# Optimization experiments

Measured on AMD Instinct MI355X. Metric: run time of the kernel, lower is better.

## Reference

```python
import jax, jax.numpy as jnp
import numpy as np


def conv1x1(x, W, b):
    # 1x1 Conv2d == per-pixel linear over channels. x: [B,C,H,W], W: [O,C], b: [O]
    return jnp.einsum('oc,bchw->bohw', W, x) + b[None, :, None, None]


def setup_inputs() -> dict:
    key = jax.random.key(0)
    ks = jax.random.split(key, 18)
    B, C, Hd, H, W = 16, 64, 64, 32, 32
    s = 0.05
    f = jax.random.normal
    return {
        'h': f(ks[0], (B, C, H, W), jnp.float32),
        'm': f(ks[1], (B, C, H, W), jnp.float32),
        'Wq': f(ks[2], (Hd, C), jnp.float32) * s,
        'bq': f(ks[3], (Hd,), jnp.float32) * s,
        'Wk': f(ks[4], (Hd, C), jnp.float32) * s,
        'bk': f(ks[5], (Hd,), jnp.float32) * s,
        'Wk2': f(ks[6], (Hd, C), jnp.float32) * s,
        'bk2': f(ks[7], (Hd,), jnp.float32) * s,
        'Wv': f(ks[8], (C, C), jnp.float32) * s,
        'bv': f(ks[9], (C,), jnp.float32) * s,
        'Wv2': f(ks[10], (C, C), jnp.float32) * s,
        'bv2': f(ks[11], (C,), jnp.float32) * s,
        'Wz': f(ks[12], (2 * C, 2 * C), jnp.float32) * s,
        'bz': f(ks[13], (2 * C,), jnp.float32) * s,
        'Wm': f(ks[14], (3 * C, 3 * C), jnp.float32) * s,
        'bm': f(ks[15], (3 * C,), jnp.float32) * s,
    }


def reference(h, m, Wq, bq, Wk, bk, Wk2, bk2, Wv, bv, Wv2, bv2, Wz, bz, Wm, bm):
    B, C, H, W = h.shape
    Hd = Wq.shape[0]
    N = H * W
    # Shared query from h
    Q_h = conv1x1(h, Wq, bq).reshape(B, Hd, N).transpose(0, 2, 1)  # [B,N,Hd]
    # Self-attention branch over h
    K_h = conv1x1(h, Wk, bk).reshape(B, Hd, N)                     # [B,Hd,N]
    A_h = jax.nn.softmax(jnp.einsum('bnd,bdm->bnm', Q_h, K_h), axis=-1)  # [B,N,N]
    V_h = conv1x1(h, Wv, bv).reshape(B, C, N)                      # [B,C,N]
    Z_h = jnp.einsum('bnm,bcm->bcn', A_h, V_h).reshape(B, C, H, W)
    # Cross-attention branch over memory m (same query Q_h)
    K_m = conv1x1(m, Wk2, bk2).reshape(B, Hd, N)
    A_m = jax.nn.softmax(jnp.einsum('bnd,bdm->bnm', Q_h, K_m), axis=-1)
    V_m = conv1x1(m, Wv2, bv2).reshape(B, C, N)
    Z_m = jnp.einsum('bnm,bcm->bcn', A_m, V_m).reshape(B, C, H, W)
    # Fuse and gated memory update
    Z = conv1x1(jnp.concatenate([Z_h, Z_m], axis=1), Wz, bz)       # [B,2C,H,W]
    combined = conv1x1(jnp.concatenate([Z, h], axis=1), Wm, bm)    # [B,3C,H,W]
    mo, mg, mi = combined[:, :C], combined[:, C:2 * C], combined[:, 2 * C:]
    mi = jax.nn.sigmoid(mi)
    new_m = (1 - mi) * m + mi * jnp.tanh(mg)
    new_h = jax.nn.sigmoid(mo) * new_m
    return (new_h, new_m)
```

## Files before the change

kernel.cpp:

```cpp
#include <hip/hip_runtime.h>

typedef unsigned short u16;
typedef unsigned int u32;
typedef __attribute__((ext_vector_type(8))) short bf16x8;
typedef __attribute__((ext_vector_type(4))) float f32x4;

#define MFMA(a, b, c) __builtin_amdgcn_mfma_f32_16x16x32_bf16((a), (b), (c), 0, 0, 0)

static __device__ __forceinline__ u16 f2bf(float x) {
  u32 u = __float_as_uint(x);
  u += 0x7FFFu + ((u >> 16) & 1u);
  return (u16)(u >> 16);
}
static __device__ __forceinline__ u16 f2bf_t(float x) {
  return (u16)(__float_as_uint(x) >> 16);
}

__global__ void prep_kernel(const float* __restrict__ Wq, const float* __restrict__ Wk,
                            const float* __restrict__ Wk2, const float* __restrict__ Wv,
                            const float* __restrict__ Wv2, const float* __restrict__ Wz,
                            const float* __restrict__ Wm, const float* __restrict__ bm,
                            u16* __restrict__ W5, u16* __restrict__ Wzb,
                            u16* __restrict__ Wmb, float* __restrict__ bmp) {
  const int id = blockIdx.x * 256 + threadIdx.x;
  if (id < 20480) {
    const int wi = id >> 12, e = id & 4095;
    const float* src = wi == 0 ? Wq : wi == 1 ? Wk : wi == 2 ? Wk2 : wi == 3 ? Wv : Wv2;
    W5[id] = f2bf(src[e]);
  } else if (id < 36864) {
    const int e = id - 20480;
    Wzb[e] = f2bf(Wz[e]);
  } else if (id < 73728) {
    const int e = id - 36864;
    const int p = e / 192, k = e % 192;
    const int hb2 = p / 96, r1 = p % 96, ctl = r1 / 48, r2 = r1 % 48;
    const int g = r2 >> 4, mm = r2 & 15;
    const int o = g * 64 + (hb2 * 2 + ctl) * 16 + mm;
    Wmb[p * 192 + k] = f2bf(Wm[o * 192 + k]);
  } else if (id < 73920) {
    const int p = id - 73728;
    const int hb2 = p / 96, r1 = p % 96, ctl = r1 / 48, r2 = r1 % 48;
    const int g = r2 >> 4, mm = r2 & 15;
    const int o = g * 64 + (hb2 * 2 + ctl) * 16 + mm;
    bmp[p] = bm[o];
  }
}

__global__ __launch_bounds__(256) void proj_kernel(
    const float* __restrict__ h, const float* __restrict__ m_,
    const float* __restrict__ bq, const float* __restrict__ bk,
    const float* __restrict__ bk2, const float* __restrict__ bv,
    const float* __restrict__ bv2, const u16* __restrict__ W5,
    u16* __restrict__ Qb, u16* __restrict__ Khb, u16* __restrict__ Kmb,
    u16* __restrict__ Vhb, u16* __restrict__ Vmb, u16* __restrict__ hbuf)
{
  const int b = blockIdx.y, n0 = blockIdx.x * 64, z = blockIdx.z;
  __shared__ __align__(16) u16 xt[64][72];
  __shared__ __align__(16) u16 st[64][72];
  const int tid = threadIdx.x;
  const float* __restrict__ X = z ? m_ : h;

  {
    const int px = tid & 63, c0 = tid >> 6;
#pragma unroll
    for (int i = 0; i < 16; ++i) {
      const int c = c0 * 16 + i;
      xt[px][c] = f2bf(X[(b * 64 + c) * 1024 + n0 + px]);
    }
  }
  __syncthreads();

  const int lane = tid & 63, w = tid >> 6;
  const int mm = lane & 15, q = lane >> 4;

  const bf16x8 xa0 = *(const bf16x8*)&xt[w * 16 + mm][q * 8];
  const bf16x8 xa1 = *(const bf16x8*)&xt[w * 16 + mm][32 + q * 8];

  auto gemm_tile = [&](const u16* Wb, const float* bias, int ot) -> f32x4 {
    const bf16x8 b0 = *(const bf16x8*)(Wb + (ot * 16 + mm) * 64 + q * 8);
    const bf16x8 b1 = *(const bf16x8*)(Wb + (ot * 16 + mm) * 64 + 32 + q * 8);
    const float bb = bias[ot * 16 + mm];
    f32x4 d = {bb, bb, bb, bb};
    d = MFMA(xa0, b0, d);
    d = MFMA(xa1, b1, d);
    return d;
  };

  auto store_nk = [&](u16* dst, const u16* Wb, const float* bias) {
#pragma unroll
    for (int ot = 0; ot < 4; ++ot) {
      const f32x4 d = gemm_tile(Wb, bias, ot);
#pragma unroll
      for (int r = 0; r < 4; ++r)
        dst[(b * 1024 + n0 + w * 16 + q * 4 + r) * 64 + ot * 16 + mm] = f2bf(d[r]);
    }
  };
  auto store_v = [&](const u16* Wb, const float* bias) {
#pragma unroll
    for (int ot = 0; ot < 4; ++ot) {
      const f32x4 d = gemm_tile(Wb, bias, ot);
#pragma unroll
      for (int r = 0; r < 4; ++r)
        st[ot * 16 + mm][w * 16 + q * 4 + r] = f2bf(d[r]);
    }
  };

  if (z == 0) {
    store_nk(Qb, W5, bq);
    store_nk(Khb, W5 + 4096, bk);
    store_v(W5 + 3 * 4096, bv);
    const int px = tid >> 2, sg = tid & 3;
    u32* dst = (u32*)(hbuf + (b * 1024 + n0 + px) * 64 + sg * 16);
    const u16* srcr = &xt[px][sg * 16];
#pragma unroll
    for (int j = 0; j < 8; ++j) dst[j] = *(const u32*)(srcr + 2 * j);
  } else {
    store_nk(Kmb, W5 + 2 * 4096, bk2);
    store_v(W5 + 4 * 4096, bv2);
  }
  __syncthreads();
  {
    u16* Vdst = z ? Vmb : Vhb;
    const int c = tid >> 2, sg = tid & 3;
    u32* dst = (u32*)(Vdst + (b * 64 + c) * 1024 + n0 + sg * 16);
    const u16* srcr = &st[c][sg * 16];
#pragma unroll
    for (int j = 0; j < 8; ++j) dst[j] = *(const u32*)(srcr + 2 * j);
  }
}

__global__ __launch_bounds__(256) void attn_kernel(
    const u16* __restrict__ Qb, const u16* __restrict__ Khb,
    const u16* __restrict__ Kmb, const u16* __restrict__ Vhb,
    const u16* __restrict__ Vmb, u16* __restrict__ Ztb)
{
  const int id = blockIdx.x;
  const int b = id & 15, rest = id >> 4;
  const int br = rest & 1, qb0 = (rest >> 1) * 64;
  const u16* __restrict__ K = br ? Kmb : Khb;
  const u16* __restrict__ V = br ? Vmb : Vhb;

  __shared__ __align__(16) u16 ps[4][16][40];
  __shared__ __align__(16) u16 zcb[4][64][66];
  __shared__ __align__(16) float rsw[4][64];

  const int tid = threadIdx.x, w = tid >> 6, lane = tid & 63;
  const int mm = lane & 15, q = lane >> 4;

  bf16x8 qa0[4], qa1[4];
#pragma unroll
  for (int qt = 0; qt < 4; ++qt) {
    const u16* Qp = Qb + (b * 1024 + qb0 + qt * 16 + mm) * 64;
    qa0[qt] = *(const bf16x8*)(Qp + q * 8);
    qa1[qt] = *(const bf16x8*)(Qp + 32 + q * 8);
  }

  f32x4 z[4][4];
#pragma unroll
  for (int qt = 0; qt < 4; ++qt)
#pragma unroll
    for (int ct = 0; ct < 4; ++ct) z[qt][ct] = (f32x4){0.f, 0.f, 0.f, 0.f};
  float rp[4][4];
#pragma unroll
  for (int qt = 0; qt < 4; ++qt)
#pragma unroll
    for (int r = 0; r < 4; ++r) rp[qt][r] = 0.f;

  const int kb0 = w * 256;
  for (int ch = 0; ch < 8; ++ch) {
    const int kb = kb0 + ch * 32;
    bf16x8 kf0[2], kf1[2];
#pragma unroll
    for (int t = 0; t < 2; ++t) {
      const u16* Kp = K + (b * 1024 + kb + t * 16 + mm) * 64;
      kf0[t] = *(const bf16x8*)(Kp + q * 8);
      kf1[t] = *(const bf16x8*)(Kp + 32 + q * 8);
    }
    bf16x8 vf[4];
#pragma unroll
    for (int ct = 0; ct < 4; ++ct)
      vf[ct] = *(const bf16x8*)(V + (b * 64 + ct * 16 + mm) * 1024 + kb + q * 8);

#pragma unroll
    for (int qt = 0; qt < 4; ++qt) {
#pragma unroll
      for (int t = 0; t < 2; ++t) {
        f32x4 s = {0.f, 0.f, 0.f, 0.f};
        s = MFMA(qa0[qt], kf0[t], s);
        s = MFMA(qa1[qt], kf1[t], s);
#pragma unroll
        for (int r = 0; r < 4; ++r) {
          const float e = __expf(s[r]);
          rp[qt][r] += e;
          ps[w][q * 4 + r][t * 16 + mm] = f2bf_t(e);
        }
      }
      const bf16x8 pa = *(const bf16x8*)&ps[w][mm][q * 8];
#pragma unroll
      for (int ct = 0; ct < 4; ++ct) z[qt][ct] = MFMA(pa, vf[ct], z[qt][ct]);
    }
  }

#pragma unroll
  for (int qt = 0; qt < 4; ++qt)
#pragma unroll
    for (int r = 0; r < 4; ++r) {
      float v = rp[qt][r];
      v += __shfl_xor(v, 1);
      v += __shfl_xor(v, 2);
      v += __shfl_xor(v, 4);
      v += __shfl_xor(v, 8);
      rp[qt][r] = v;
    }

#pragma unroll
  for (int qt = 0; qt < 4; ++qt) {
#pragma unroll
    for (int ct = 0; ct < 4; ++ct)
#pragma unroll
      for (int r = 0; r < 4; ++r)
        zcb[w][qt * 16 + q * 4 + r][ct * 16 + mm] = f2bf_t(z[qt][ct][r]);
    if (mm == 0) {
#pragma unroll
      for (int r = 0; r < 4; ++r) rsw[w][qt * 16 + q * 4 + r] = rp[qt][r];
    }
  }
  __syncthreads();

  const int c2 = tid & 31, q0 = tid >> 5;
#pragma unroll
  for (int i = 0; i < 8; ++i) {
    const int query = q0 + i * 8;
    const float rt = rsw[0][query] + rsw[1][query] + rsw[2][query] + rsw[3][query];
    const float rinv = __builtin_amdgcn_rcpf(rt);
    float vlo = 0.f, vhi = 0.f;
#pragma unroll
    for (int ww = 0; ww < 4; ++ww) {
      const u32 u = *(const u32*)&zcb[ww][query][c2 * 2];
      vlo += __uint_as_float(u << 16);
      vhi += __uint_as_float(u & 0xffff0000u);
    }
    vlo *= rinv;
    vhi *= rinv;
    const u32 o = __builtin_amdgcn_perm(__float_as_uint(vhi), __float_as_uint(vlo),
                                        0x07060302u);
    *(u32*)(Ztb + (b * 1024 + qb0 + query) * 128 + br * 64 + c2 * 2) = o;
  }
}

__global__ __launch_bounds__(256) void tail_kernel(
    const u16* __restrict__ Ztb, const u16* __restrict__ hbuf,
    const float* __restrict__ m_, const u16* __restrict__ Wzb,
    const float* __restrict__ bz, const u16* __restrict__ Wmb,
    const float* __restrict__ bmp, float* __restrict__ out)
{
  const int b = blockIdx.y, n0 = blockIdx.x * 32;
  __shared__ __align__(16) u16 zp[32][136];
  const int tid = threadIdx.x, lane = tid & 63, wv = tid >> 6;
  const int mm = lane & 15, q = lane >> 4;
  const int pxt = wv & 1, oh = wv >> 1;

  {
    bf16x8 za[4];
#pragma unroll
    for (int ks = 0; ks < 4; ++ks)
      za[ks] = *(const bf16x8*)(Ztb + (b * 1024 + n0 + pxt * 16 + mm) * 128 +
                                ks * 32 + q * 8);
#pragma unroll
    for (int ot = 0; ot < 4; ++ot) {
      const int o = oh * 64 + ot * 16 + mm;
      const float bb = bz[o];
      f32x4 d = {bb, bb, bb, bb};
#pragma unroll
      for (int ks = 0; ks < 4; ++ks) {
        const bf16x8 wb = *(const bf16x8*)(Wzb + o * 128 + ks * 32 + q * 8);
        d = MFMA(za[ks], wb, d);
      }
#pragma unroll
      for (int r = 0; r < 4; ++r) zp[pxt * 16 + q * 4 + r][o] = f2bf(d[r]);
    }
  }
  __syncthreads();

  {
    const int hb2 = oh;
    bf16x8 fa[6];
#pragma unroll
    for (int ks = 0; ks < 4; ++ks)
      fa[ks] = *(const bf16x8*)&zp[pxt * 16 + mm][ks * 32 + q * 8];
    {
      const u16* hp = hbuf + (b * 1024 + n0 + pxt * 16 + mm) * 64;
      fa[4] = *(const bf16x8*)(hp + q * 8);
      fa[5] = *(const bf16x8*)(hp + 32 + q * 8);
    }
    f32x4 dd[6];
#pragma unroll
    for (int j = 0; j < 6; ++j) {
      const int p = hb2 * 96 + j * 16 + mm;
      const float bb = bmp[p];
      f32x4 d = {bb, bb, bb, bb};
#pragma unroll
      for (int ks = 0; ks < 6; ++ks) {
        const bf16x8 wb = *(const bf16x8*)(Wmb + p * 192 + ks * 32 + q * 8);
        d = MFMA(fa[ks], wb, d);
      }
      dd[j] = d;
    }
#pragma unroll
    for (int ctl = 0; ctl < 2; ++ctl) {
      const int c = (hb2 * 2 + ctl) * 16 + mm;
      const int px = n0 + pxt * 16 + q * 4;
      const float4 mold = *(const float4*)(m_ + (b * 64 + c) * 1024 + px);
      float4 nh, nm;
#pragma unroll
      for (int r = 0; r < 4; ++r) {
        const float xo = dd[ctl * 3 + 0][r];
        const float xg = dd[ctl * 3 + 1][r];
        const float xi = dd[ctl * 3 + 2][r];
        const float si = __builtin_amdgcn_rcpf(1.f + __expf(-xi));
        const float th = 1.f - 2.f * __builtin_amdgcn_rcpf(__expf(2.f * xg) + 1.f);
        const float so = __builtin_amdgcn_rcpf(1.f + __expf(-xo));
        const float mo = ((const float*)&mold)[r];
        const float nmv = (1.f - si) * mo + si * th;
        ((float*)&nm)[r] = nmv;
        ((float*)&nh)[r] = so * nmv;
      }
      *(float4*)(out + (b * 64 + c) * 1024 + px) = nh;
      *(float4*)(out + 1048576 + (b * 64 + c) * 1024 + px) = nm;
    }
  }
}

extern "C" void kernel_launch(void* const* d_in, const int* in_sizes, int n_in,
                              void* d_out, int out_size, void* d_ws, size_t ws_size,
                              hipStream_t stream) {
  const float* h   = (const float*)d_in[0];
  const float* m   = (const float*)d_in[1];
  const float* Wq  = (const float*)d_in[2];
  const float* bq  = (const float*)d_in[3];
  const float* Wk  = (const float*)d_in[4];
  const float* bk  = (const float*)d_in[5];
  const float* Wk2 = (const float*)d_in[6];
  const float* bk2 = (const float*)d_in[7];
  const float* Wv  = (const float*)d_in[8];
  const float* bv  = (const float*)d_in[9];
  const float* Wv2 = (const float*)d_in[10];
  const float* bv2 = (const float*)d_in[11];
  const float* Wz  = (const float*)d_in[12];
  const float* bz  = (const float*)d_in[13];
  const float* Wm  = (const float*)d_in[14];
  const float* bm  = (const float*)d_in[15];
  float* out = (float*)d_out;

  char* ws = (char*)d_ws;
  const size_t MB = 1024 * 1024;
  u16* Qb   = (u16*)(ws + 0 * MB);
  u16* Khb  = (u16*)(ws + 2 * MB);
  u16* Kmb  = (u16*)(ws + 4 * MB);
  u16* Vhb  = (u16*)(ws + 6 * MB);
  u16* Vmb  = (u16*)(ws + 8 * MB);
  u16* hbuf = (u16*)(ws + 10 * MB);
  u16* Ztb  = (u16*)(ws + 12 * MB);
  u16* W5   = (u16*)(ws + 16 * MB);
  u16* Wzb  = (u16*)(ws + 16 * MB + 40960);
  u16* Wmb  = (u16*)(ws + 16 * MB + 73728);
  float* bmp = (float*)(ws + 16 * MB + 147456);

  prep_kernel<<<289, 256, 0, stream>>>(Wq, Wk, Wk2, Wv, Wv2, Wz, Wm, bm,
                                       W5, Wzb, Wmb, bmp);
  proj_kernel<<<dim3(16, 16, 2), 256, 0, stream>>>(h, m, bq, bk, bk2, bv, bv2, W5,
                                                   Qb, Khb, Kmb, Vhb, Vmb, hbuf);
  attn_kernel<<<512, 256, 0, stream>>>(Qb, Khb, Kmb, Vhb, Vmb, Ztb);
  tail_kernel<<<dim3(32, 16), 256, 0, stream>>>(Ztb, hbuf, m, Wzb, bz, Wmb, bmp, out);
}
```

Measured before the change: 140.8 us.

## Swap MFMA operand order, pass P via shuffles, halve attention query tile

The attention kernel now computes S^T by swapping MFMA operands, packs exp values to bf16 pairs and rearranges them into the PV operand with cross-lane shuffles instead of an LDS round trip. It also halves the query tile per block to 32, doubling the grid and adding a launch-bounds occupancy hint. Projection and tail kernels also swap operand order so results come out in rows they can store as packed vector writes directly, which removes the V staging LDS buffer and a barrier. Smaller query tiles mean K/V chunks are reloaded by twice as many blocks, and the shuffles add some ALU work.

```diff
diff --git a/kernel.cpp b/kernel.cpp
--- a/kernel.cpp
+++ b/kernel.cpp
@@ -12,8 +12,11 @@
   u += 0x7FFFu + ((u >> 16) & 1u);
   return (u16)(u >> 16);
 }
-static __device__ __forceinline__ u16 f2bf_t(float x) {
-  return (u16)(__float_as_uint(x) >> 16);
+static __device__ __forceinline__ u32 packbf_t(float hi, float lo) {
+  return __builtin_amdgcn_perm(__float_as_uint(hi), __float_as_uint(lo), 0x07060302u);
+}
+static __device__ __forceinline__ u32 packbf(float lo, float hi) {
+  return (u32)f2bf(lo) | ((u32)f2bf(hi) << 16);
 }
 
 __global__ void prep_kernel(const float* __restrict__ Wq, const float* __restrict__ Wk,
@@ -56,16 +59,17 @@
 {
   const int b = blockIdx.y, n0 = blockIdx.x * 64, z = blockIdx.z;
   __shared__ __align__(16) u16 xt[64][72];
-  __shared__ __align__(16) u16 st[64][72];
   const int tid = threadIdx.x;
   const float* __restrict__ X = z ? m_ : h;
 
   {
-    const int px = tid & 63, c0 = tid >> 6;
-#pragma unroll
-    for (int i = 0; i < 16; ++i) {
-      const int c = c0 * 16 + i;
-      xt[px][c] = f2bf(X[(b * 64 + c) * 1024 + n0 + px]);
+    const int px = tid & 63, c0 = (tid >> 6) * 16;
+#pragma unroll
+    for (int i = 0; i < 8; ++i) {
+      const int c = c0 + 2 * i;
+      const float f0 = X[(b * 64 + c) * 1024 + n0 + px];
+      const float f1 = X[(b * 64 + c + 1) * 1024 + n0 + px];
+      *(u32*)&xt[px][c] = packbf(f0, f1);
     }
   }
   __syncthreads();
@@ -76,160 +80,157 @@
   const bf16x8 xa0 = *(const bf16x8*)&xt[w * 16 + mm][q * 8];
   const bf16x8 xa1 = *(const bf16x8*)&xt[w * 16 + mm][32 + q * 8];
 
-  auto gemm_tile = [&](const u16* Wb, const float* bias, int ot) -> f32x4 {
-    const bf16x8 b0 = *(const bf16x8*)(Wb + (ot * 16 + mm) * 64 + q * 8);
-    const bf16x8 b1 = *(const bf16x8*)(Wb + (ot * 16 + mm) * 64 + 32 + q * 8);
-    const float bb = bias[ot * 16 + mm];
-    f32x4 d = {bb, bb, bb, bb};
-    d = MFMA(xa0, b0, d);
-    d = MFMA(xa1, b1, d);
-    return d;
+  auto qk_store = [&](u16* dst, const u16* Wb, const float* bias) {
+#pragma unroll
+    for (int ot = 0; ot < 4; ++ot) {
+      const bf16x8 wb0 = *(const bf16x8*)(Wb + (ot * 16 + mm) * 64 + q * 8);
+      const bf16x8 wb1 = *(const bf16x8*)(Wb + (ot * 16 + mm) * 64 + 32 + q * 8);
+      const float4 b4 = *(const float4*)(bias + ot * 16 + q * 4);
+      f32x4 d = {b4.x, b4.y, b4.z, b4.w};
+      d = MFMA(wb0, xa0, d);
+      d = MFMA(wb1, xa1, d);
+      uint2 val;
+      val.x = packbf(d[0], d[1]);
+      val.y = packbf(d[2], d[3]);
+      *(uint2*)(dst + (b * 1024 + n0 + w * 16 + mm) * 64 + ot * 16 + q * 4) = val;
+    }
   };
-
-  auto store_nk = [&](u16* dst, const u16* Wb, const float* bias) {
+  auto v_store = [&](u16* dst, const u16* Wb, const float* bias) {
 #pragma unroll
     for (int ot = 0; ot < 4; ++ot) {
-      const f32x4 d = gemm_tile(Wb, bias, ot);
-#pragma unroll
-      for (int r = 0; r < 4; ++r)
-        dst[(b * 1024 + n0 + w * 16 + q * 4 + r) * 64 + ot * 16 + mm] = f2bf(d[r]);
+      const bf16x8 wb0 = *(const bf16x8*)(Wb + (ot * 16 + mm) * 64 + q * 8);
+      const bf16x8 wb1 = *(const bf16x8*)(Wb + (ot * 16 + mm) * 64 + 32 + q * 8);
+      const float bb = bias[ot * 16 + mm];
+      f32x4 d = {bb, bb, bb, bb};
+      d = MFMA(xa0, wb0, d);
+      d = MFMA(xa1, wb1, d);
+      uint2 val;
+      val.x = packbf(d[0], d[1]);
+      val.y = packbf(d[2], d[3]);
+      *(uint2*)(dst + (b * 64 + ot * 16 + mm) * 1024 + n0 + w * 16 + q * 4) = val;
     }
   };
-  auto store_v = [&](const u16* Wb, const float* bias) {
-#pragma unroll
-    for (int ot = 0; ot < 4; ++ot) {
-      const f32x4 d = gemm_tile(Wb, bias, ot);
-#pragma unroll
-      for (int r = 0; r < 4; ++r)
-        st[ot * 16 + mm][w * 16 + q * 4 + r] = f2bf(d[r]);
-    }
-  };
 
   if (z == 0) {
-    store_nk(Qb, W5, bq);
-    store_nk(Khb, W5 + 4096, bk);
-    store_v(W5 + 3 * 4096, bv);
+    qk_store(Qb, W5, bq);
+    qk_store(Khb, W5 + 4096, bk);
+    v_store(Vhb, W5 + 3 * 4096, bv);
     const int px = tid >> 2, sg = tid & 3;
     u32* dst = (u32*)(hbuf + (b * 1024 + n0 + px) * 64 + sg * 16);
     const u16* srcr = &xt[px][sg * 16];
 #pragma unroll
     for (int j = 0; j < 8; ++j) dst[j] = *(const u32*)(srcr + 2 * j);
   } else {
-    store_nk(Kmb, W5 + 2 * 4096, bk2);
-    store_v(W5 + 4 * 4096, bv2);
-  }
-  __syncthreads();
-  {
-    u16* Vdst = z ? Vmb : Vhb;
-    const int c = tid >> 2, sg = tid & 3;
-    u32* dst = (u32*)(Vdst + (b * 64 + c) * 1024 + n0 + sg * 16);
-    const u16* srcr = &st[c][sg * 16];
-#pragma unroll
-    for (int j = 0; j < 8; ++j) dst[j] = *(const u32*)(srcr + 2 * j);
-  }
-}
-
-__global__ __launch_bounds__(256) void attn_kernel(
+    qk_store(Kmb, W5 + 2 * 4096, bk2);
+    v_store(Vmb, W5 + 4 * 4096, bv2);
+  }
+}
+
+__global__ __launch_bounds__(256, 4) void attn_kernel(
     const u16* __restrict__ Qb, const u16* __restrict__ Khb,
     const u16* __restrict__ Kmb, const u16* __restrict__ Vhb,
     const u16* __restrict__ Vmb, u16* __restrict__ Ztb)
 {
   const int id = blockIdx.x;
   const int b = id & 15, rest = id >> 4;
-  const int br = rest & 1, qb0 = (rest >> 1) * 64;
+  const int br = rest & 1, qb0 = (rest >> 1) * 32;
   const u16* __restrict__ K = br ? Kmb : Khb;
   const u16* __restrict__ V = br ? Vmb : Vhb;
 
-  __shared__ __align__(16) u16 ps[4][16][40];
-  __shared__ __align__(16) u16 zcb[4][64][66];
-  __shared__ __align__(16) float rsw[4][64];
+  __shared__ __align__(16) u16 zcb[4][32][68];
+  __shared__ float rsw[4][32];
 
   const int tid = threadIdx.x, w = tid >> 6, lane = tid & 63;
   const int mm = lane & 15, q = lane >> 4;
 
-  bf16x8 qa0[4], qa1[4];
-#pragma unroll
-  for (int qt = 0; qt < 4; ++qt) {
+  bf16x8 qa0[2], qa1[2];
+#pragma unroll
+  for (int qt = 0; qt < 2; ++qt) {
     const u16* Qp = Qb + (b * 1024 + qb0 + qt * 16 + mm) * 64;
     qa0[qt] = *(const bf16x8*)(Qp + q * 8);
     qa1[qt] = *(const bf16x8*)(Qp + 32 + q * 8);
   }
 
-  f32x4 z[4][4];
-#pragma unroll
-  for (int qt = 0; qt < 4; ++qt)
+  f32x4 z[2][4];
+#pragma unroll
+  for (int qt = 0; qt < 2; ++qt)
 #pragma unroll
     for (int ct = 0; ct < 4; ++ct) z[qt][ct] = (f32x4){0.f, 0.f, 0.f, 0.f};
-  float rp[4][4];
-#pragma unroll
-  for (int qt = 0; qt < 4; ++qt)
-#pragma unroll
-    for (int r = 0; r < 4; ++r) rp[qt][r] = 0.f;
+  float rp[2] = {0.f, 0.f};
 
   const int kb0 = w * 256;
+  const int base = (2 * (q & 1)) * 16 + mm;
+  const bool hiq = q >= 2;
+
   for (int ch = 0; ch < 8; ++ch) {
     const int kb = kb0 + ch * 32;
-    bf16x8 kf0[2], kf1[2];
+    bf16x8 kf0[2], kf1[2], vf[4];
 #pragma unroll
     for (int t = 0; t < 2; ++t) {
       const u16* Kp = K + (b * 1024 + kb + t * 16 + mm) * 64;
       kf0[t] = *(const bf16x8*)(Kp + q * 8);
       kf1[t] = *(const bf16x8*)(Kp + 32 + q * 8);
     }
-    bf16x8 vf[4];
 #pragma unroll
     for (int ct = 0; ct < 4; ++ct)
       vf[ct] = *(const bf16x8*)(V + (b * 64 + ct * 16 + mm) * 1024 + kb + q * 8);
 
 #pragma unroll
-    for (int qt = 0; qt < 4; ++qt) {
-#pragma unroll
-      for (int t = 0; t < 2; ++t) {
+    for (int qt = 0; qt < 2; ++qt) {
+      u32 P0, P1, P2, P3;
+      {
         f32x4 s = {0.f, 0.f, 0.f, 0.f};
-        s = MFMA(qa0[qt], kf0[t], s);
-        s = MFMA(qa1[qt], kf1[t], s);
-#pragma unroll
-        for (int r = 0; r < 4; ++r) {
-          const float e = __expf(s[r]);
-          rp[qt][r] += e;
-          ps[w][q * 4 + r][t * 16 + mm] = f2bf_t(e);
-        }
-      }
-      const bf16x8 pa = *(const bf16x8*)&ps[w][mm][q * 8];
-#pragma unroll
-      for (int ct = 0; ct < 4; ++ct) z[qt][ct] = MFMA(pa, vf[ct], z[qt][ct]);
-    }
-  }
-
-#pragma unroll
-  for (int qt = 0; qt < 4; ++qt)
-#pragma unroll
-    for (int r = 0; r < 4; ++r) {
-      float v = rp[qt][r];
-      v += __shfl_xor(v, 1);
-      v += __shfl_xor(v, 2);
-      v += __shfl_xor(v, 4);
-      v += __shfl_xor(v, 8);
-      rp[qt][r] = v;
-    }
-
-#pragma unroll
-  for (int qt = 0; qt < 4; ++qt) {
-#pragma unroll
-    for (int ct = 0; ct < 4; ++ct)
-#pragma unroll
-      for (int r = 0; r < 4; ++r)
-        zcb[w][qt * 16 + q * 4 + r][ct * 16 + mm] = f2bf_t(z[qt][ct][r]);
-    if (mm == 0) {
-#pragma unroll
-      for (int r = 0; r < 4; ++r) rsw[w][qt * 16 + q * 4 + r] = rp[qt][r];
-    }
+        s = MFMA(kf0[0], qa0[qt], s);
+        s = MFMA(kf1[0], qa1[qt], s);
+        const float e0 = __expf(s[0]), e1 = __expf(s[1]);
+        const float e2 = __expf(s[2]), e3 = __expf(s[3]);
+        rp[qt] += (e0 + e1) + (e2 + e3);
+        P0 = packbf_t(e1, e0);
+        P1 = packbf_t(e3, e2);
+      }
+      {
+        f32x4 s = {0.f, 0.f, 0.f, 0.f};
+        s = MFMA(kf0[1], qa0[qt], s);
+        s = MFMA(kf1[1], qa1[qt], s);
+        const float e0 = __expf(s[0]), e1 = __expf(s[1]);
+        const float e2 = __expf(s[2]), e3 = __expf(s[3]);
+        rp[qt] += (e0 + e1) + (e2 + e3);
+        P2 = packbf_t(e1, e0);
+        P3 = packbf_t(e3, e2);
+      }
+      const u32 l0 = (u32)__shfl((int)P0, base),      h0 = (u32)__shfl((int)P2, base);
+      const u32 l1 = (u32)__shfl((int)P1, base),      h1 = (u32)__shfl((int)P3, base);
+      const u32 l2 = (u32)__shfl((int)P0, base + 16), h2 = (u32)__shfl((int)P2, base + 16);
+      const u32 l3 = (u32)__shfl((int)P1, base + 16), h3 = (u32)__shfl((int)P3, base + 16);
+      union { u32 u[4]; bf16x8 v; } bu;
+      bu.u[0] = hiq ? h0 : l0;
+      bu.u[1] = hiq ? h1 : l1;
+      bu.u[2] = hiq ? h2 : l2;
+      bu.u[3] = hiq ? h3 : l3;
+#pragma unroll
+      for (int ct = 0; ct < 4; ++ct) z[qt][ct] = MFMA(vf[ct], bu.v, z[qt][ct]);
+    }
+  }
+
+#pragma unroll
+  for (int qt = 0; qt < 2; ++qt) {
+#pragma unroll
+    for (int ct = 0; ct < 4; ++ct) {
+      uint2 val;
+      val.x = packbf_t(z[qt][ct][1], z[qt][ct][0]);
+      val.y = packbf_t(z[qt][ct][3], z[qt][ct][2]);
+      *(uint2*)&zcb[w][qt * 16 + mm][ct * 16 + q * 4] = val;
+    }
+    float v = rp[qt];
+    v += __shfl_xor(v, 16);
+    v += __shfl_xor(v, 32);
+    if (q == 0) rsw[w][qt * 16 + mm] = v;
   }
   __syncthreads();
 
   const int c2 = tid & 31, q0 = tid >> 5;
 #pragma unroll
-  for (int i = 0; i < 8; ++i) {
+  for (int i = 0; i < 4; ++i) {
     const int query = q0 + i * 8;
     const float rt = rsw[0][query] + rsw[1][query] + rsw[2][query] + rsw[3][query];
     const float rinv = __builtin_amdgcn_rcpf(rt);
@@ -242,9 +243,7 @@
     }
     vlo *= rinv;
     vhi *= rinv;
-    const u32 o = __builtin_amdgcn_perm(__float_as_uint(vhi), __float_as_uint(vlo),
-                                        0x07060302u);
-    *(u32*)(Ztb + (b * 1024 + qb0 + query) * 128 + br * 64 + c2 * 2) = o;
+    *(u32*)(Ztb + (b * 1024 + qb0 + query) * 128 + br * 64 + c2 * 2) = packbf_t(vhi, vlo);
   }
 }
 
@@ -268,16 +267,18 @@
                                 ks * 32 + q * 8);
 #pragma unroll
     for (int ot = 0; ot < 4; ++ot) {
-      const int o = oh * 64 + ot * 16 + mm;
-      const float bb = bz[o];
-      f32x4 d = {bb, bb, bb, bb};
+      const int o0 = oh * 64 + ot * 16;
+      const float4 b4 = *(const float4*)(bz + o0 + q * 4);
+      f32x4 d = {b4.x, b4.y, b4.z, b4.w};
 #pragma unroll
       for (int ks = 0; ks < 4; ++ks) {
-        const bf16x8 wb = *(const bf16x8*)(Wzb + o * 128 + ks * 32 + q * 8);
-        d = MFMA(za[ks], wb, d);
-      }
-#pragma unroll
-      for (int r = 0; r < 4; ++r) zp[pxt * 16 + q * 4 + r][o] = f2bf(d[r]);
+        const bf16x8 wb = *(const bf16x8*)(Wzb + (o0 + mm) * 128 + ks * 32 + q * 8);
+        d = MFMA(wb, za[ks], d);
+      }
+      uint2 val;
+      val.x = packbf(d[0], d[1]);
+      val.y = packbf(d[2], d[3]);
+      *(uint2*)&zp[pxt * 16 + mm][o0 + q * 4] = val;
     }
   }
   __syncthreads();
@@ -370,6 +371,6 @@
                                        W5, Wzb, Wmb, bmp);
   proj_kernel<<<dim3(16, 16, 2), 256, 0, stream>>>(h, m, bq, bk, bk2, bv, bv2, W5,
                                                    Qb, Khb, Kmb, Vhb, Vmb, hbuf);
-  attn_kernel<<<512, 256, 0, stream>>>(Qb, Khb, Kmb, Vhb, Vmb, Ztb);
+  attn_kernel<<<1024, 256, 0, stream>>>(Qb, Khb, Kmb, Vhb, Vmb, Ztb);
   tail_kernel<<<dim3(32, 16), 256, 0, stream>>>(Ztb, hbuf, m, Wzb, bz, Wmb, bmp, out);
 }
```

New measurement: 157.7 us. 1.12x slower.
